# Kernel optimization log

Measured on AMD Instinct MI355X. Metric: run time of the kernel, lower is better.

The kernel has to match this reference:

```python
import jax, jax.numpy as jnp
import numpy as np
from jax import lax

B, T, G = 64, 256, 66            # batch, seq_len, label_alphabet_size + 2 (START/STOP)
DC, DW, DL, DI = 128, 256, 128, 128   # char/word/lexi/intent emb dims
HC = 384                          # cnn_hidden_dim (= DW + DL so q.k dims match)
LH = 512                          # lstm_hidden_dim (bidirectional: 256 per direction)
NL = 2                            # lstm layers
VC, VW, VL, VI = 5000, 30000, 20000, 50
START, STOP = G - 2, G - 1
TEMP = float(np.sqrt(DC))         # ScaledDotProductAttention temperature = char_emb_dim**0.5
H4 = 4 * (LH // 2)


def setup_inputs() -> dict:
    key = jax.random.key(0)
    ks = jax.random.split(key, 16)
    s = 0.02
    inp = {
        'batch_word': jax.random.randint(ks[0], (B, T), 0, VW),
        'batch_intents': jax.random.randint(ks[1], (B, 1), 0, VI),
        'batch_wordlen': jnp.full((B,), T, dtype=jnp.int32),
        'batch_char': jax.random.randint(ks[2], (B, T), 0, VC),
        'batch_charlen': jnp.full((B,), T, dtype=jnp.int32),
        'mask': jnp.ones((B, T), dtype=bool),
        'batch_lexi': jax.random.randint(ks[3], (B, T), 0, VL),
        'batch_label': jax.random.randint(ks[4], (B, T), 0, G - 2),
        'char_emb': jax.random.normal(ks[5], (VC, DC)) * s,
        'word_emb': jax.random.normal(ks[6], (VW, DW)) * s,
        'lexi_emb': jax.random.normal(ks[7], (VL, DL)) * s,
        'intent_emb': jax.random.normal(ks[8], (VI, DI)) * s,
        'conv_w': jax.random.normal(ks[9], (HC, DC, 3)) * s,
        'conv_b': jnp.zeros((HC,)),
        'lstm_w_ih': jax.random.normal(ks[10], (NL, 2, H4, LH)) * s,
        'lstm_w_hh': jax.random.normal(ks[11], (NL, 2, H4, LH // 2)) * s,
        'lstm_b_ih': jnp.zeros((NL, 2, H4)),
        'lstm_b_hh': jnp.zeros((NL, 2, H4)),
        'proj_w': jax.random.normal(ks[12], (G, LH)) * s,
        'proj_b': jnp.zeros((G,)),
    }
    trans = jax.random.normal(ks[13], (G, G)) * 0.1
    trans = trans.at[:, START].set(-10000.0).at[STOP, :].set(-10000.0)
    inp['transitions'] = trans
    return inp


def _lstm_dir(x, w_ih, w_hh, b_ih, b_hh, reverse):
    # x: [B,T,D] -> [B,T,H]; PyTorch gate order i,f,g,o
    xs = jnp.swapaxes(x, 0, 1)            # [T,B,D]
    if reverse:
        xs = xs[::-1]
    pre = xs @ w_ih.T + (b_ih + b_hh)     # [T,B,4H]
    H = w_hh.shape[1]
    h0 = jnp.zeros((x.shape[0], H), x.dtype)

    def step(carry, p):
        h, c = carry
        g = p + h @ w_hh.T
        i, f, gg, o = jnp.split(g, 4, axis=-1)
        c = jax.nn.sigmoid(f) * c + jax.nn.sigmoid(i) * jnp.tanh(gg)
        h = jax.nn.sigmoid(o) * jnp.tanh(c)
        return (h, c), h

    _, hs = lax.scan(step, (h0, h0), pre)
    if reverse:
        hs = hs[::-1]
    return jnp.swapaxes(hs, 0, 1)


def _emissions(batch_word, batch_intents, batch_char, batch_lexi,
               char_emb, word_emb, lexi_emb, intent_emb, conv_w, conv_b,
               lstm_w_ih, lstm_w_hh, lstm_b_ih, lstm_b_hh, proj_w, proj_b):
    ce = char_emb[batch_char]                             # [B,T,DC]
    conv = lax.conv_general_dilated(jnp.swapaxes(ce, 1, 2), conv_w, (1,), [(1, 1)],
                                    dimension_numbers=('NCH', 'OIH', 'NCH'))
    char_cnn = jnp.swapaxes(conv + conv_b[None, :, None], 1, 2)   # [B,T,HC]
    ie = intent_emb[batch_intents[:, 0]][:, None, :]      # [B,1,DI]
    ie_t = jnp.broadcast_to(ie, (ce.shape[0], ce.shape[1], DI))   # repeat_interleave over time
    q = jnp.concatenate([char_cnn, ie_t], -1)             # [B,T,512] char features
    kv = jnp.concatenate([word_emb[batch_word], lexi_emb[batch_lexi], ie_t], -1)  # [B,T,512]
    attn = jax.nn.softmax(jnp.einsum('bqd,bkd->bqk', q, kv) / TEMP, axis=-1)
    x = jnp.einsum('bqk,bkd->bqd', attn, kv)              # [B,T,512]
    for l in range(NL):
        fwd = _lstm_dir(x, lstm_w_ih[l, 0], lstm_w_hh[l, 0], lstm_b_ih[l, 0], lstm_b_hh[l, 0], False)
        bwd = _lstm_dir(x, lstm_w_ih[l, 1], lstm_w_hh[l, 1], lstm_b_ih[l, 1], lstm_b_hh[l, 1], True)
        x = jnp.concatenate([fwd, bwd], -1)               # [B,T,LH]
    return x @ proj_w.T + proj_b                          # [B,T,G]


def _crf_nll(emit, mask, tags, trans):
    # NCRF++ forward algorithm: alpha_j(t)=lse_i(alpha_i(t-1)+trans[i,j])+emit[t,j]
    m = mask.astype(emit.dtype)
    alpha0 = trans[START][None, :] + emit[:, 0]           # [B,G]

    def step(alpha, xs):
        e_t, m_t = xs
        a_new = jax.nn.logsumexp(alpha[:, :, None] + trans[None], axis=1) + e_t
        return jnp.where(m_t[:, None] > 0, a_new, alpha), None

    alpha, _ = lax.scan(step, alpha0, (jnp.swapaxes(emit, 0, 1)[1:], jnp.swapaxes(m, 0, 1)[1:]))
    logZ = jax.nn.logsumexp(alpha + trans[:, STOP][None], axis=1)  # [B]
    bidx = jnp.arange(emit.shape[0])
    e_gold = jnp.take_along_axis(emit, tags[:, :, None], axis=2)[:, :, 0]  # [B,T]
    t_gold = trans[tags[:, :-1], tags[:, 1:]]             # [B,T-1]
    lens = mask.sum(1).astype(jnp.int32)
    last_tag = tags[bidx, lens - 1]
    gold = (trans[START, tags[:, 0]] + (e_gold * m).sum(1)
            + (t_gold * m[:, 1:]).sum(1) + trans[last_tag, STOP])
    return (logZ - gold).sum()


def _viterbi(emit, trans):
    # full-length sequences (mask all ones)
    Bb = emit.shape[0]
    delta0 = trans[START][None] + emit[:, 0]

    def step(delta, e_t):
        s = delta[:, :, None] + trans[None]               # [B,G_from,G_to]
        return jnp.max(s, axis=1) + e_t, jnp.argmax(s, axis=1)

    delta, bps = lax.scan(step, delta0, jnp.swapaxes(emit, 0, 1)[1:])  # bps: [T-1,B,G]
    last = jnp.argmax(delta + trans[:, STOP][None], axis=1)            # [B]
    bidx = jnp.arange(Bb)

    def back(tag, bp_t):
        return bp_t[bidx, tag], tag

    first, tags_rev = lax.scan(back, last, bps, reverse=True)
    tags = jnp.concatenate([first[None], tags_rev], 0)    # [T,B]
    return jnp.swapaxes(tags, 0, 1)                       # [B,T]


def reference(batch_word, batch_intents, batch_wordlen, batch_char, batch_charlen,
              mask, batch_lexi, batch_label,
              char_emb, word_emb, lexi_emb, intent_emb, conv_w, conv_b,
              lstm_w_ih, lstm_w_hh, lstm_b_ih, lstm_b_hh, proj_w, proj_b, transitions):
    emit = _emissions(batch_word, batch_intents, batch_char, batch_lexi,
                      char_emb, word_emb, lexi_emb, intent_emb, conv_w, conv_b,
                      lstm_w_ih, lstm_w_hh, lstm_b_ih, lstm_b_hh, proj_w, proj_b)
    total_loss = _crf_nll(emit, mask, batch_label, transitions)
    tag_seq = _viterbi(emit, transitions)
    return total_loss, tag_seq
```

## Files before the change

kernel.cpp:

```cpp
#include <hip/hip_runtime.h>

#define NB 64
#define NT 256
#define BT 16384
#define NG 66
#define START_ 64
#define STOP_ 65
#define INV_TEMP 0.08838834764831845f

typedef _Float16 half2_t __attribute__((ext_vector_type(2)));
typedef _Float16 h8 __attribute__((ext_vector_type(8)));
typedef float f4x __attribute__((ext_vector_type(4)));
union H2U { unsigned u; half2_t h; };
typedef const __attribute__((address_space(1))) void* gptr_t;
typedef __attribute__((address_space(3))) void* sptr_t;

#define OFF_PREF   0L
#define OFF_CEPADH 0L
#define OFF_QH     1056768L
#define OFF_SC     5251072L
#define OFF_PH     9445376L
#define OFF_KVT    11542528L
#define OFF_PREB   16777216L
#define OFF_KVH    16777216L
#define OFF_X1H    33554432L
#define OFF_YH     37748736L
#define OFF_WT     41943040L
#define OFF_WIH    42467328L
#define OFF_PROJW  43515904L
#define OFF_W2H    43532800L
#define OFF_EMIT   43606528L

__device__ __forceinline__ float fsig(float x) {
    return 1.f / (1.f + __expf(-x));
}
__device__ __forceinline__ float ftanh(float x) {
    float xc = fminf(fmaxf(x, -15.f), 15.f);
    float e = __expf(2.f * xc);
    return (e - 1.f) / (e + 1.f);
}
__device__ __forceinline__ uint2 f4h(float4 v) {
    H2U a, b;
    a.h[0] = (_Float16)v.x; a.h[1] = (_Float16)v.y;
    b.h[0] = (_Float16)v.z; b.h[1] = (_Float16)v.w;
    return make_uint2(a.u, b.u);
}

__global__ __launch_bounds__(128) void embed_k(
    const int* __restrict__ word, const int* __restrict__ intents,
    const int* __restrict__ chars, const int* __restrict__ lexi,
    const float* __restrict__ word_emb, const float* __restrict__ lexi_emb,
    const float* __restrict__ intent_emb, const float* __restrict__ char_emb,
    _Float16* __restrict__ kvh, _Float16* __restrict__ qh, _Float16* __restrict__ cepad)
{
    int bt = blockIdx.x;
    int b = bt >> 8, t = bt & 255;
    int tid = threadIdx.x;
    const float4* wrow = (const float4*)(word_emb + (long)word[bt] * 256);
    const float4* lrow = (const float4*)(lexi_emb + (long)lexi[bt] * 128);
    const float4* irow = (const float4*)(intent_emb + (long)intents[b] * 128);
    const float4* crow = (const float4*)(char_emb + (long)chars[bt] * 128);
    uint2* kvrow = (uint2*)(kvh + (long)bt * 512);
    uint2* qrow  = (uint2*)(qh + (long)bt * 512);
    uint2* cerow = (uint2*)(cepad + ((long)b * 258 + t + 1) * 128);
    if (tid < 64)       kvrow[tid] = f4h(wrow[tid]);
    else if (tid < 96)  kvrow[tid] = f4h(lrow[tid - 64]);
    else { uint2 v = f4h(irow[tid - 96]); kvrow[tid] = v; qrow[tid] = v; }
    if (tid < 32) cerow[tid] = f4h(crow[tid]);
    if (t == 0) {
        uint2 z = make_uint2(0u, 0u);
        if (tid < 32)      ((uint2*)(cepad + (long)b * 258 * 128))[tid] = z;
        else if (tid < 64) ((uint2*)(cepad + ((long)b * 258 + 257) * 128))[tid - 32] = z;
    }
}

__global__ __launch_bounds__(256) void prep_k(const float* __restrict__ conv_w,
                                              _Float16* __restrict__ w2,
                                              float* __restrict__ out0)
{
    int idx = blockIdx.x * 256 + threadIdx.x;
    if (idx == 0) out0[0] = 0.f;
    if (idx < 384 * 384) {
        int o = idx / 384, r = idx % 384;
        int k = r >> 7, c = r & 127;
        w2[o * 384 + r] = (_Float16)conv_w[o * 384 + c * 3 + k];
    }
}

__global__ __launch_bounds__(256) void cvt_k(const float* __restrict__ src,
                                             uint2* __restrict__ dst)
{
    long i = ((long)blockIdx.x * 256 + threadIdx.x);
    dst[i] = f4h(((const float4*)src)[i]);
}

__global__ __launch_bounds__(256) void wt_k(const float* __restrict__ whh,
                                            uint2* __restrict__ wt)
{
    int bid = blockIdx.x;
    int ld = bid >> 6;
    int rt = (bid >> 2) & 15;
    int kt = bid & 3;
    const float* src = whh + ((long)ld * 1024 + rt * 64) * 256 + kt * 64;
    __shared__ float tile[64][65];
    int c = threadIdx.x & 63, r0 = threadIdx.x >> 6;
#pragma unroll
    for (int i = 0; i < 16; i++)
        tile[r0 + i * 4][c] = src[(long)(r0 + i * 4) * 256 + c];
    __syncthreads();
    uint2* dst = wt + (long)ld * 65536;
#pragma unroll
    for (int i = 0; i < 4; i++) {
        int kql = r0 + i * 4;
        H2U ua, ub;
        ua.h[0] = (_Float16)tile[c][4 * kql + 0];
        ua.h[1] = (_Float16)tile[c][4 * kql + 1];
        ub.h[0] = (_Float16)tile[c][4 * kql + 2];
        ub.h[1] = (_Float16)tile[c][4 * kql + 3];
        dst[(long)(kt * 16 + kql) * 1024 + rt * 64 + c] = make_uint2(ua.u, ub.u);
    }
}

__global__ __launch_bounds__(256) void tr_k(const _Float16* __restrict__ kv,
                                            _Float16* __restrict__ kvT)
{
    int bid = blockIdx.x;
    int b = bid >> 5, rem = bid & 31;
    int dt = rem >> 2, tt = rem & 3;
    __shared__ _Float16 tile[64][66];
    int c = threadIdx.x & 63, r0 = threadIdx.x >> 6;
    const _Float16* src = kv + ((long)b * 256 + tt * 64) * 512 + dt * 64;
#pragma unroll
    for (int i = 0; i < 16; i++)
        tile[r0 + i * 4][c] = src[(long)(r0 + i * 4) * 512 + c];
    __syncthreads();
    _Float16* dst = kvT + ((long)b * 512 + dt * 64) * 256 + tt * 64;
#pragma unroll
    for (int i = 0; i < 16; i++)
        dst[(long)(r0 + i * 4) * 256 + c] = tile[c][r0 + i * 4];
}

__global__ __launch_bounds__(256) void hgemm_k(
    const _Float16* __restrict__ A, int K, long sA, int amode,
    const _Float16* __restrict__ Bm, long sB, int N,
    void* __restrict__ Cv, long sC, int ldc, int c_half,
    const float* __restrict__ bias0, const float* __restrict__ bias1, float alpha)
{
    A  += (long)blockIdx.z * sA;
    Bm += (long)blockIdx.z * sB;
    const long cbase = (long)blockIdx.z * sC;
    const int m0 = blockIdx.x * 128, n0 = blockIdx.y * 128;
    const int tid = threadIdx.x;
    const int lane = tid & 63, wave = tid >> 6;
    const int wm = (wave & 1) * 64, wn = (wave >> 1) * 64;
    __shared__ _Float16 As[128][32];
    __shared__ _Float16 Bs[128][32];
    f4x acc[4][4];
#pragma unroll
    for (int i = 0; i < 4; i++)
#pragma unroll
        for (int j = 0; j < 4; j++) acc[i][j] = (f4x){0.f, 0.f, 0.f, 0.f};

    const int rl = lane >> 2;
    const int ck = lane & 3;
    const int fm = lane & 15, fq = lane >> 4;
    const int ar0 = m0 + wave * 32 + rl;
    const int ar1 = ar0 + 16;
    const long aof0 = amode ? ((long)ar0 * 128 + (long)(ar0 >> 8) * 256) : ((long)ar0 * K);
    const long aof1 = amode ? ((long)ar1 * 128 + (long)(ar1 >> 8) * 256) : ((long)ar1 * K);
    int br0 = n0 + wave * 32 + rl;
    int br1 = br0 + 16;
    if (br0 >= N) br0 = N - 1;
    if (br1 >= N) br1 = N - 1;

    for (int k0 = 0; k0 < K; k0 += 32) {
        __builtin_amdgcn_global_load_lds((gptr_t)(A + aof0 + k0 + ck * 8),
                                         (sptr_t)(&As[wave * 32][0]), 16, 0, 0);
        __builtin_amdgcn_global_load_lds((gptr_t)(A + aof1 + k0 + ck * 8),
                                         (sptr_t)(&As[wave * 32 + 16][0]), 16, 0, 0);
        __builtin_amdgcn_global_load_lds((gptr_t)(Bm + (long)br0 * K + k0 + ck * 8),
                                         (sptr_t)(&Bs[wave * 32][0]), 16, 0, 0);
        __builtin_amdgcn_global_load_lds((gptr_t)(Bm + (long)br1 * K + k0 + ck * 8),
                                         (sptr_t)(&Bs[wave * 32 + 16][0]), 16, 0, 0);
        __syncthreads();
        h8 af[4], bf[4];
#pragma unroll
        for (int i = 0; i < 4; i++) af[i] = *(const h8*)&As[wm + i * 16 + fm][fq * 8];
#pragma unroll
        for (int i = 0; i < 4; i++) bf[i] = *(const h8*)&Bs[wn + i * 16 + fm][fq * 8];
#pragma unroll
        for (int i = 0; i < 4; i++)
#pragma unroll
            for (int j = 0; j < 4; j++)
                acc[i][j] = __builtin_amdgcn_mfma_f32_16x16x32_f16(af[i], bf[j], acc[i][j], 0, 0, 0);
        __syncthreads();
    }
    const int col = lane & 15, rowb = (lane >> 4) * 4;
#pragma unroll
    for (int i = 0; i < 4; i++) {
#pragma unroll
        for (int j = 0; j < 4; j++) {
            int n = n0 + wn + j * 16 + col;
            if (n < N) {
                float bsum = (bias0 ? bias0[n] : 0.f) + (bias1 ? bias1[n] : 0.f);
#pragma unroll
                for (int r = 0; r < 4; r++) {
                    int m = m0 + wm + i * 16 + rowb + r;
                    float v = acc[i][j][r] * alpha + bsum;
                    if (c_half) ((_Float16*)Cv)[cbase + (long)m * ldc + n] = (_Float16)v;
                    else        ((float*)Cv)[cbase + (long)m * ldc + n] = v;
                }
            }
        }
    }
}

__global__ __launch_bounds__(256) void softmax_k(const float* __restrict__ scores,
                                                 _Float16* __restrict__ P)
{
    int row = blockIdx.x * 4 + (threadIdx.x >> 6);
    int lane = threadIdx.x & 63;
    const float4* p = (const float4*)(scores + (long)row * 256);
    float4 v = p[lane];
    float m = fmaxf(fmaxf(v.x, v.y), fmaxf(v.z, v.w));
#pragma unroll
    for (int off = 32; off; off >>= 1) m = fmaxf(m, __shfl_xor(m, off));
    v.x = __expf(v.x - m); v.y = __expf(v.y - m);
    v.z = __expf(v.z - m); v.w = __expf(v.w - m);
    float s = v.x + v.y + v.z + v.w;
#pragma unroll
    for (int off = 32; off; off >>= 1) s += __shfl_xor(s, off);
    float inv = 1.f / s;
    v.x *= inv; v.y *= inv; v.z *= inv; v.w *= inv;
    ((uint2*)(P + (long)row * 256))[lane] = f4h(v);
}

__global__ __launch_bounds__(512, 2) void lstm_k(
    const float* __restrict__ preF, const float* __restrict__ preB,
    const uint4* __restrict__ wtL,
    _Float16* __restrict__ out)
{
    const int dir = blockIdx.x & 1;
    const int b   = blockIdx.x >> 1;
    const int tid = threadIdx.x;
    const int r0  = tid * 2;
    __shared__ uint4 wlds[16][512];
    __shared__ __align__(16) _Float16 hq16[256];
    __shared__ float gl[1024];
    const float* pre = (dir ? preB : preF) + (long)b * 256 * 1024;
    const uint4* W = wtL + (long)dir * 32768;

    uint4 wreg[40];
#pragma unroll
    for (int i = 0; i < 40; i++) wreg[i] = W[i * 512 + tid];
#pragma unroll
    for (int i = 0; i < 16; i++) wlds[i][tid] = W[(40 + i) * 512 + tid];
    float cst = 0.f;
    __syncthreads();

#define DOT(WV, HV) do {                                                         \
    H2U wx, wy, wz, ww, hx, hy;                                                  \
    wx.u = (WV).x; wy.u = (WV).y; wz.u = (WV).z; ww.u = (WV).w;                  \
    hx.u = (HV).x; hy.u = (HV).y;                                                \
    a0 = __builtin_amdgcn_fdot2(wx.h, hx.h, a0, false);                          \
    a0 = __builtin_amdgcn_fdot2(wy.h, hy.h, a0, false);                          \
    a1 = __builtin_amdgcn_fdot2(wz.h, hx.h, a1, false);                          \
    a1 = __builtin_amdgcn_fdot2(ww.h, hy.h, a1, false);                          \
} while (0)

    for (int t = 0; t < 256; t++) {
        const int tpre = dir ? (255 - t) : t;
        float2 p = *(const float2*)(pre + (long)tpre * 1024 + r0);
        float a0 = 0.f, a1 = 0.f;
        if (t > 0) {
            uint4 s0[8];
#pragma unroll
            for (int i = 0; i < 8; i++) s0[i] = W[(56 + i) * 512 + tid];
#pragma unroll
            for (int i = 0; i < 20; i++) {
                uint4 h4 = *(const uint4*)&hq16[i * 8];
                uint2 ha = make_uint2(h4.x, h4.y), hb = make_uint2(h4.z, h4.w);
                DOT(wreg[2 * i], ha);
                DOT(wreg[2 * i + 1], hb);
            }
#pragma unroll
            for (int i = 0; i < 8; i++) {
                uint4 h4 = *(const uint4*)&hq16[(40 + 2 * i) * 4];
                uint2 ha = make_uint2(h4.x, h4.y), hb = make_uint2(h4.z, h4.w);
                uint4 w0 = wlds[2 * i][tid];
                uint4 w1 = wlds[2 * i + 1][tid];
                DOT(w0, ha);
                DOT(w1, hb);
            }
#pragma unroll
            for (int i = 0; i < 4; i++) {
                uint4 h4 = *(const uint4*)&hq16[(56 + 2 * i) * 4];
                uint2 ha = make_uint2(h4.x, h4.y), hb = make_uint2(h4.z, h4.w);
                DOT(s0[2 * i], ha);
                DOT(s0[2 * i + 1], hb);
            }
        }
        *(float2*)&gl[r0] = make_float2(a0 + p.x, a1 + p.y);
        __syncthreads();
        if (tid < 256) {
            const int j = tid;
            float gi = gl[j], gf = gl[256 + j], gg = gl[512 + j], go = gl[768 + j];
            float si = fsig(gi), sf = fsig(gf), so = fsig(go);
            cst = sf * cst + si * ftanh(gg);
            float h = so * ftanh(cst);
            _Float16 hh = (_Float16)h;
            hq16[j] = hh;
            out[((long)b * 256 + tpre) * 512 + dir * 256 + j] = hh;
        }
        __syncthreads();
    }
#undef DOT
}

__global__ __launch_bounds__(128) void crf_k(
    const float* __restrict__ emit, const float* __restrict__ trans,
    const int* __restrict__ labels, float* __restrict__ outv)
{
    const int b = blockIdx.x & 63;
    const bool vit = blockIdx.x >= 64;
    const int tid = threadIdx.x;
    __shared__ float Tl[NG * NG];
    __shared__ __align__(16) float bufA[68];
    __shared__ __align__(16) float bufB[68];
    __shared__ unsigned char bp[256][NG];
    __shared__ float redv[128];
    for (int i = tid; i < NG * NG; i += 128) Tl[i] = trans[i];
    __syncthreads();
    const float* eb = emit + (long)b * 256 * NG;

    float tcol[68];
    if (tid < NG) {
#pragma unroll
        for (int i = 0; i < NG; i++) tcol[i] = Tl[i * NG + tid];
    }
    tcol[66] = 0.f; tcol[67] = 0.f;
    if (tid < NG) bufA[tid] = Tl[START_ * NG + tid] + eb[tid];
    if (tid == 66 || tid == 67) { bufA[tid] = -1e30f; bufB[tid] = -1e30f; }
    __syncthreads();

    if (!vit) {
        for (int t = 1; t < 256; t++) {
            const float* prev = (t & 1) ? bufA : bufB;
            float* cur  = (t & 1) ? bufB : bufA;
            float e_t = (tid < NG) ? eb[t * NG + tid] : 0.f;
            if (tid < NG) {
                float pv[68];
#pragma unroll
                for (int c = 0; c < 17; c++) {
                    float4 p4 = *(const float4*)&prev[c * 4];
                    pv[c * 4 + 0] = p4.x + tcol[c * 4 + 0];
                    pv[c * 4 + 1] = p4.y + tcol[c * 4 + 1];
                    pv[c * 4 + 2] = p4.z + tcol[c * 4 + 2];
                    pv[c * 4 + 3] = p4.w + tcol[c * 4 + 3];
                }
                float m0 = -1e30f, m1 = -1e30f, m2 = -1e30f, m3 = -1e30f;
#pragma unroll
                for (int c = 0; c < 17; c++) {
                    m0 = fmaxf(m0, pv[c * 4 + 0]);
                    m1 = fmaxf(m1, pv[c * 4 + 1]);
                    m2 = fmaxf(m2, pv[c * 4 + 2]);
                    m3 = fmaxf(m3, pv[c * 4 + 3]);
                }
                float m = fmaxf(fmaxf(m0, m1), fmaxf(m2, m3));
                float s0 = 0.f, s1 = 0.f, s2 = 0.f, s3 = 0.f;
#pragma unroll
                for (int c = 0; c < 17; c++) {
                    s0 += __expf(pv[c * 4 + 0] - m);
                    s1 += __expf(pv[c * 4 + 1] - m);
                    s2 += __expf(pv[c * 4 + 2] - m);
                    s3 += __expf(pv[c * 4 + 3] - m);
                }
                cur[tid] = m + __logf((s0 + s1) + (s2 + s3)) + e_t;
            }
            __syncthreads();
        }
        const int* lab = labels + b * 256;
        float g = 0.f;
        for (int t = tid; t < 256; t += 128) g += eb[t * NG + lab[t]];
        for (int t = tid; t < 255; t += 128) g += Tl[lab[t] * NG + lab[t + 1]];
        redv[tid] = g;
        __syncthreads();
        if (tid == 0) {
            float* fin = bufB;
            float m = -1e30f;
            for (int j = 0; j < NG; j++) m = fmaxf(m, fin[j] + Tl[j * NG + STOP_]);
            float s = 0.f;
            for (int j = 0; j < NG; j++) s += __expf(fin[j] + Tl[j * NG + STOP_] - m);
            float logZ = m + __logf(s);
            float gold = Tl[START_ * NG + lab[0]] + Tl[lab[255] * NG + STOP_];
            for (int i = 0; i < 128; i++) gold += redv[i];
            atomicAdd(outv, logZ - gold);
        }
    } else {
        for (int t = 1; t < 256; t++) {
            const float* prev = (t & 1) ? bufA : bufB;
            float* cur  = (t & 1) ? bufB : bufA;
            float e_t = (tid < NG) ? eb[t * NG + tid] : 0.f;
            if (tid < NG) {
                float m = -1e30f; int arg = 0;
#pragma unroll
                for (int c = 0; c < 17; c++) {
                    float4 p4 = *(const float4*)&prev[c * 4];
                    float v0 = p4.x + tcol[c * 4 + 0];
                    float v1 = p4.y + tcol[c * 4 + 1];
                    float v2 = p4.z + tcol[c * 4 + 2];
                    float v3 = p4.w + tcol[c * 4 + 3];
                    if (v0 > m) { m = v0; arg = c * 4 + 0; }
                    if (v1 > m) { m = v1; arg = c * 4 + 1; }
                    if (v2 > m) { m = v2; arg = c * 4 + 2; }
                    if (v3 > m) { m = v3; arg = c * 4 + 3; }
                }
                bp[t][tid] = (unsigned char)arg;
                cur[tid] = m + e_t;
            }
            __syncthreads();
        }
        if (tid == 0) {
            float* fin = bufB;
            float m = -1e30f; int tag = 0;
            for (int j = 0; j < NG; j++) {
                float v = fin[j] + Tl[j * NG + STOP_];
                if (v > m) { m = v; tag = j; }
            }
            float* od = outv + 1 + (long)b * 256;
            od[255] = (float)tag;
            for (int t = 255; t >= 1; t--) { tag = bp[t][tag]; od[t - 1] = (float)tag; }
        }
    }
}

extern "C" void kernel_launch(void* const* d_in, const int* in_sizes, int n_in,
                              void* d_out, int out_size, void* d_ws, size_t ws_size,
                              hipStream_t stream)
{
    const int*   batch_word    = (const int*)d_in[0];
    const int*   batch_intents = (const int*)d_in[1];
    const int*   batch_char    = (const int*)d_in[3];
    const int*   batch_lexi    = (const int*)d_in[6];
    const int*   batch_label   = (const int*)d_in[7];
    const float* char_emb      = (const float*)d_in[8];
    const float* word_emb      = (const float*)d_in[9];
    const float* lexi_emb      = (const float*)d_in[10];
    const float* intent_emb    = (const float*)d_in[11];
    const float* conv_w        = (const float*)d_in[12];
    const float* conv_b        = (const float*)d_in[13];
    const float* w_ih          = (const float*)d_in[14];
    const float* w_hh          = (const float*)d_in[15];
    const float* b_ih          = (const float*)d_in[16];
    const float* b_hh          = (const float*)d_in[17];
    const float* proj_w        = (const float*)d_in[18];
    const float* proj_b        = (const float*)d_in[19];
    const float* trans         = (const float*)d_in[20];
    float* out = (float*)d_out;
    float* ws  = (float*)d_ws;

    float*    preF   = ws + OFF_PREF;
    float*    preB   = ws + OFF_PREB;
    float*    scores = ws + OFF_SC;
    float*    emit   = ws + OFF_EMIT;
    _Float16* cepadh = (_Float16*)(ws + OFF_CEPADH);
    _Float16* qh     = (_Float16*)(ws + OFF_QH);
    _Float16* Ph     = (_Float16*)(ws + OFF_PH);
    _Float16* kvTh   = (_Float16*)(ws + OFF_KVT);
    _Float16* kvh    = (_Float16*)(ws + OFF_KVH);
    _Float16* x1h    = (_Float16*)(ws + OFF_X1H);
    _Float16* yh     = (_Float16*)(ws + OFF_YH);
    uint2*    wt_u2  = (uint2*)(ws + OFF_WT);
    _Float16* wihh   = (_Float16*)(ws + OFF_WIH);
    _Float16* projwh = (_Float16*)(ws + OFF_PROJW);
    _Float16* w2h    = (_Float16*)(ws + OFF_W2H);

    embed_k<<<BT, 128, 0, stream>>>(batch_word, batch_intents, batch_char, batch_lexi,
                                    word_emb, lexi_emb, intent_emb, char_emb,
                                    kvh, qh, cepadh);
    prep_k<<<(384 * 384 + 255) / 256, 256, 0, stream>>>(conv_w, w2h, out);
    wt_k<<<256, 256, 0, stream>>>(w_hh, wt_u2);
    cvt_k<<<2048, 256, 0, stream>>>(w_ih, (uint2*)wihh);
    cvt_k<<<33, 256, 0, stream>>>(proj_w, (uint2*)projwh);
    tr_k<<<2048, 256, 0, stream>>>(kvh, kvTh);

    hgemm_k<<<dim3(128, 3, 1), 256, 0, stream>>>(
        cepadh, 384, 0L, 1, w2h, 0L, 384,
        qh, 0L, 512, 1, conv_b, nullptr, 1.f);
    hgemm_k<<<dim3(2, 2, NB), 256, 0, stream>>>(
        qh, 512, 131072L, 0, kvh, 131072L, 256,
        scores, 65536L, 256, 0, nullptr, nullptr, INV_TEMP);
    softmax_k<<<4096, 256, 0, stream>>>(scores, Ph);
    hgemm_k<<<dim3(2, 4, NB), 256, 0, stream>>>(
        Ph, 256, 65536L, 0, kvTh, 131072L, 512,
        x1h, 131072L, 512, 1, nullptr, nullptr, 1.f);

    for (int l = 0; l < 2; l++) {
        const _Float16* xin = l ? yh : x1h;
        _Float16* xout = l ? x1h : yh;
        for (int d = 0; d < 2; d++) {
            hgemm_k<<<dim3(128, 8, 1), 256, 0, stream>>>(
                xin, 512, 0L, 0, wihh + (long)(l * 2 + d) * 1024 * 512, 0L, 1024,
                d ? preB : preF, 0L, 1024, 0,
                b_ih + (l * 2 + d) * 1024, b_hh + (l * 2 + d) * 1024, 1.f);
        }
        lstm_k<<<128, 512, 0, stream>>>(preF, preB,
                                        (const uint4*)(wt_u2 + (long)l * 2 * 65536), xout);
    }

    hgemm_k<<<dim3(128, 1, 1), 256, 0, stream>>>(
        x1h, 512, 0L, 0, projwh, 0L, NG,
        emit, 0L, NG, 0, proj_b, nullptr, 1.f);
    crf_k<<<128, 128, 0, stream>>>(emit, trans, batch_label, out);
}
```

Baseline: 1.599 ms.

## Split CRF forward/Viterbi reductions across 4 lanes per tag, drop START/STOP states

```diff
diff --git a/kernel.cpp b/kernel.cpp
--- a/kernel.cpp
+++ b/kernel.cpp
@@ -317,115 +317,108 @@
 #undef DOT
 }
 
-__global__ __launch_bounds__(128) void crf_k(
+__global__ __launch_bounds__(256) void crf_k(
     const float* __restrict__ emit, const float* __restrict__ trans,
     const int* __restrict__ labels, float* __restrict__ outv)
 {
     const int b = blockIdx.x & 63;
     const bool vit = blockIdx.x >= 64;
     const int tid = threadIdx.x;
+    const int j = tid >> 2;
+    const int s = tid & 3;
     __shared__ float Tl[NG * NG];
-    __shared__ __align__(16) float bufA[68];
-    __shared__ __align__(16) float bufB[68];
-    __shared__ unsigned char bp[256][NG];
-    __shared__ float redv[128];
-    for (int i = tid; i < NG * NG; i += 128) Tl[i] = trans[i];
+    __shared__ __align__(16) float bufA[64];
+    __shared__ __align__(16) float bufB[64];
+    __shared__ unsigned char bp[256][64];
+    __shared__ float redv[256];
+    for (int i = tid; i < NG * NG; i += 256) Tl[i] = trans[i];
     __syncthreads();
     const float* eb = emit + (long)b * 256 * NG;
 
-    float tcol[68];
-    if (tid < NG) {
-#pragma unroll
-        for (int i = 0; i < NG; i++) tcol[i] = Tl[i * NG + tid];
-    }
-    tcol[66] = 0.f; tcol[67] = 0.f;
-    if (tid < NG) bufA[tid] = Tl[START_ * NG + tid] + eb[tid];
-    if (tid == 66 || tid == 67) { bufA[tid] = -1e30f; bufB[tid] = -1e30f; }
+    float tcol[16];
+#pragma unroll
+    for (int k = 0; k < 16; k++) tcol[k] = Tl[(s * 16 + k) * NG + j];
+    if (s == 0) bufA[j] = Tl[START_ * NG + j] + eb[j];
     __syncthreads();
 
     if (!vit) {
         for (int t = 1; t < 256; t++) {
             const float* prev = (t & 1) ? bufA : bufB;
             float* cur  = (t & 1) ? bufB : bufA;
-            float e_t = (tid < NG) ? eb[t * NG + tid] : 0.f;
-            if (tid < NG) {
-                float pv[68];
-#pragma unroll
-                for (int c = 0; c < 17; c++) {
-                    float4 p4 = *(const float4*)&prev[c * 4];
-                    pv[c * 4 + 0] = p4.x + tcol[c * 4 + 0];
-                    pv[c * 4 + 1] = p4.y + tcol[c * 4 + 1];
-                    pv[c * 4 + 2] = p4.z + tcol[c * 4 + 2];
-                    pv[c * 4 + 3] = p4.w + tcol[c * 4 + 3];
-                }
-                float m0 = -1e30f, m1 = -1e30f, m2 = -1e30f, m3 = -1e30f;
-#pragma unroll
-                for (int c = 0; c < 17; c++) {
-                    m0 = fmaxf(m0, pv[c * 4 + 0]);
-                    m1 = fmaxf(m1, pv[c * 4 + 1]);
-                    m2 = fmaxf(m2, pv[c * 4 + 2]);
-                    m3 = fmaxf(m3, pv[c * 4 + 3]);
-                }
-                float m = fmaxf(fmaxf(m0, m1), fmaxf(m2, m3));
-                float s0 = 0.f, s1 = 0.f, s2 = 0.f, s3 = 0.f;
-#pragma unroll
-                for (int c = 0; c < 17; c++) {
-                    s0 += __expf(pv[c * 4 + 0] - m);
-                    s1 += __expf(pv[c * 4 + 1] - m);
-                    s2 += __expf(pv[c * 4 + 2] - m);
-                    s3 += __expf(pv[c * 4 + 3] - m);
-                }
-                cur[tid] = m + __logf((s0 + s1) + (s2 + s3)) + e_t;
-            }
+            float pv[16];
+#pragma unroll
+            for (int c = 0; c < 4; c++) {
+                float4 p4 = *(const float4*)&prev[s * 16 + c * 4];
+                pv[c * 4 + 0] = p4.x + tcol[c * 4 + 0];
+                pv[c * 4 + 1] = p4.y + tcol[c * 4 + 1];
+                pv[c * 4 + 2] = p4.z + tcol[c * 4 + 2];
+                pv[c * 4 + 3] = p4.w + tcol[c * 4 + 3];
+            }
+            float m = pv[0];
+#pragma unroll
+            for (int k = 1; k < 16; k++) m = fmaxf(m, pv[k]);
+            float sum = 0.f;
+#pragma unroll
+            for (int k = 0; k < 16; k++) sum += __expf(pv[k] - m);
+#pragma unroll
+            for (int off = 1; off <= 2; off <<= 1) {
+                float mo = __shfl_xor(m, off);
+                float so = __shfl_xor(sum, off);
+                float mn = fmaxf(m, mo);
+                sum = sum * __expf(m - mn) + so * __expf(mo - mn);
+                m = mn;
+            }
+            if (s == 0) cur[j] = m + __logf(sum) + eb[t * NG + j];
             __syncthreads();
         }
         const int* lab = labels + b * 256;
-        float g = 0.f;
-        for (int t = tid; t < 256; t += 128) g += eb[t * NG + lab[t]];
-        for (int t = tid; t < 255; t += 128) g += Tl[lab[t] * NG + lab[t + 1]];
+        float g = eb[tid * NG + lab[tid]];
+        if (tid < 255) g += Tl[lab[tid] * NG + lab[tid + 1]];
         redv[tid] = g;
         __syncthreads();
         if (tid == 0) {
             float* fin = bufB;
             float m = -1e30f;
-            for (int j = 0; j < NG; j++) m = fmaxf(m, fin[j] + Tl[j * NG + STOP_]);
-            float s = 0.f;
-            for (int j = 0; j < NG; j++) s += __expf(fin[j] + Tl[j * NG + STOP_] - m);
-            float logZ = m + __logf(s);
+            for (int k = 0; k < 64; k++) m = fmaxf(m, fin[k] + Tl[k * NG + STOP_]);
+            float sz = 0.f;
+            for (int k = 0; k < 64; k++) sz += __expf(fin[k] + Tl[k * NG + STOP_] - m);
+            float logZ = m + __logf(sz);
             float gold = Tl[START_ * NG + lab[0]] + Tl[lab[255] * NG + STOP_];
-            for (int i = 0; i < 128; i++) gold += redv[i];
+            for (int i = 0; i < 256; i++) gold += redv[i];
             atomicAdd(outv, logZ - gold);
         }
     } else {
         for (int t = 1; t < 256; t++) {
             const float* prev = (t & 1) ? bufA : bufB;
             float* cur  = (t & 1) ? bufB : bufA;
-            float e_t = (tid < NG) ? eb[t * NG + tid] : 0.f;
-            if (tid < NG) {
-                float m = -1e30f; int arg = 0;
-#pragma unroll
-                for (int c = 0; c < 17; c++) {
-                    float4 p4 = *(const float4*)&prev[c * 4];
-                    float v0 = p4.x + tcol[c * 4 + 0];
-                    float v1 = p4.y + tcol[c * 4 + 1];
-                    float v2 = p4.z + tcol[c * 4 + 2];
-                    float v3 = p4.w + tcol[c * 4 + 3];
-                    if (v0 > m) { m = v0; arg = c * 4 + 0; }
-                    if (v1 > m) { m = v1; arg = c * 4 + 1; }
-                    if (v2 > m) { m = v2; arg = c * 4 + 2; }
-                    if (v3 > m) { m = v3; arg = c * 4 + 3; }
-                }
-                bp[t][tid] = (unsigned char)arg;
-                cur[tid] = m + e_t;
-            }
+            float pv[16];
+#pragma unroll
+            for (int c = 0; c < 4; c++) {
+                float4 p4 = *(const float4*)&prev[s * 16 + c * 4];
+                pv[c * 4 + 0] = p4.x + tcol[c * 4 + 0];
+                pv[c * 4 + 1] = p4.y + tcol[c * 4 + 1];
+                pv[c * 4 + 2] = p4.z + tcol[c * 4 + 2];
+                pv[c * 4 + 3] = p4.w + tcol[c * 4 + 3];
+            }
+            float m = pv[0]; int arg = s * 16;
+#pragma unroll
+            for (int k = 1; k < 16; k++)
+                if (pv[k] > m) { m = pv[k]; arg = s * 16 + k; }
+#pragma unroll
+            for (int off = 1; off <= 2; off <<= 1) {
+                float mo = __shfl_xor(m, off);
+                int ao = __shfl_xor(arg, off);
+                if (mo > m || (mo == m && ao < arg)) { m = mo; arg = ao; }
+            }
+            if (s == 0) { bp[t][j] = (unsigned char)arg; cur[j] = m + eb[t * NG + j]; }
             __syncthreads();
         }
         if (tid == 0) {
             float* fin = bufB;
             float m = -1e30f; int tag = 0;
-            for (int j = 0; j < NG; j++) {
-                float v = fin[j] + Tl[j * NG + STOP_];
-                if (v > m) { m = v; tag = j; }
+            for (int k = 0; k < 64; k++) {
+                float v = fin[k] + Tl[k * NG + STOP_];
+                if (v > m) { m = v; tag = k; }
             }
             float* od = outv + 1 + (long)b * 256;
             od[255] = (float)tag;
@@ -511,5 +504,5 @@
     hgemm_k<<<dim3(128, 1, 1), 256, 0, stream>>>(
         x1h, 512, 0L, 0, projwh, 0L, NG,
         emit, 0L, NG, 0, proj_b, nullptr, 1.f);
-    crf_k<<<128, 128, 0, stream>>>(emit, trans, batch_label, out);
-}
+    crf_k<<<128, 256, 0, stream>>>(emit, trans, batch_label, out);
+}
```

Result: faster. 1.418 ms (-11.3%).
